# Performance work log

Hardware: AMD Instinct MI355X
Metric: run time of the kernel (lower is better)

Reference implementation:

```python
import jax, jax.numpy as jnp
import numpy as np

DOT_TEMP = 0.05  # hardcoded in the original forward (self.temperature is never used)
EPS = 1e-6


def setup_inputs() -> dict:
    key = jax.random.key(0)
    k1, k2 = jax.random.split(key)
    bsz, n_views, dim = 4096, 2, 128
    features = jax.random.normal(k1, (bsz, n_views, dim), dtype=jnp.float32)
    labels = jax.random.randint(k2, (bsz,), 0, 100, dtype=jnp.int32)
    return {"features": features, "labels": labels}


def reference(features, labels):
    bsz, V, dim = features.shape  # V = n_views; contrast_mode='all' -> anchor_count = contrast_count = V
    n = V * bsz

    # contrast_feature = cat(unbind(features, dim=1), dim=0): [view0 batch; view1 batch; ...]
    cf = jnp.transpose(features, (1, 0, 2)).reshape(n, dim)  # [n, dim]

    # positive mask: eq(labels, labels.T) tiled, diagonal zeroed
    eq = labels[:, None] == labels[None, :]  # [bsz, bsz]
    mask = jnp.tile(eq.astype(jnp.float32), (V, V))  # [n, n]
    mask = mask * (1.0 - jnp.eye(n, dtype=jnp.float32))

    # Key simplification (exactly faithful): mask3[i] (eq) and mask2[i] (ne) are complementary,
    # so unique(cat(where(mask3[i]), where(mask2[i]))) == arange(n) for every row. Hence each
    # loop iteration in the original computes the SAME scalar from the full gram matrix.
    lab2 = jnp.tile(labels, V)  # matches labels2[:n] layout in the original
    diff = (lab2[:, None] != lab2[None, :]).astype(jnp.float32)  # [n, n]

    dots = jnp.matmul(cf, cf.T) / DOT_TEMP  # [n, n]
    dm = dots * diff
    maxd = jnp.max(dm, axis=1, keepdims=True)
    S = jnp.sum(jnp.exp(dm - maxd))  # exp_terms.sum() -- identical for every valid row
    N = jnp.sum(diff)                # different_label_mask.sum()

    # rows with mask2[i].sum() == 0 are skipped (left at zero)
    valid = jnp.tile(jnp.any(labels[None, :] != labels[:, None], axis=1), V)  # [n]
    xv = jnp.where(valid, S, 0.0)
    nv = jnp.where(valid, N, 0.0)

    # if not all(negtivesum == 0): x = x / negtivesum   (safe divide for skipped rows)
    all_zero = jnp.all(nv == 0.0)
    xv = jnp.where(all_zero, xv, xv / jnp.where(nv == 0.0, 1.0, nv))

    log_prob = -jnp.log(xv[:, None] + EPS)  # [n, 1], broadcast over columns
    msum = jnp.sum(mask, axis=1)
    msum_safe = jnp.where(msum == 0.0, 1.0, msum)
    pos_logits = -jnp.sum(mask * log_prob, axis=1) / msum_safe  # [n]
    loss = jnp.mean(pos_logits)  # mean over view(anchor_count, bsz) == overall mean
    return loss
```

## Files before the change

### kernel.cpp

```cpp
#include <hip/hip_runtime.h>
#include <hip/hip_bf16.h>
#include <stdint.h>

#define N_TOT 8192
#define BSZ   4096
#define NCH   32
#define SCALE2 28.853900817779268f

typedef _Float16 f16x8 __attribute__((ext_vector_type(8)));
typedef float f32x4 __attribute__((ext_vector_type(4)));

__device__ __forceinline__ float fast_exp2(float x) {
#if __has_builtin(__builtin_amdgcn_exp2f)
  return __builtin_amdgcn_exp2f(x);
#else
  return exp2f(x);
#endif
}
#define EXP2(x) fast_exp2(x)

__global__ __launch_bounds__(256) void prep13_kernel(
    const float* __restrict__ feat, const int* __restrict__ labels,
    _Float16* __restrict__ H2, unsigned char* __restrict__ lab8, int* __restrict__ cnt) {
  if (blockIdx.x == 512) {
    __shared__ int h[128];
    if (threadIdx.x < 128) h[threadIdx.x] = 0;
    __syncthreads();
    for (int i = threadIdx.x; i < BSZ; i += 256) atomicAdd(&h[labels[i] & 127], 1);
    __syncthreads();
    if (threadIdx.x < 128) cnt[threadIdx.x] = h[threadIdx.x];
    for (int i = threadIdx.x; i < N_TOT; i += 256)
      lab8[i] = (unsigned char)labels[i & (BSZ - 1)];
    return;
  }
  int idx = blockIdx.x * 256 + threadIdx.x;
  int rowblk = idx >> 8, inner = idx & 255;
  int k8 = inner >> 4, rlo = inner & 15;
  int r = rowblk * 16 + rlo;
  int b = r & (BSZ - 1), v = r >> 12;
  const float* src = feat + ((size_t)((b << 1) + v) << 7) + k8 * 8;
  float4 x0 = *(const float4*)src;
  float4 x1 = *(const float4*)(src + 4);
  float xs[8] = {x0.x, x0.y, x0.z, x0.w, x1.x, x1.y, x1.z, x1.w};
  f16x8 hv;
#pragma unroll
  for (int j = 0; j < 8; ++j) hv[j] = (_Float16)xs[j];
  *(f16x8*)((char*)H2 + (size_t)idx * 16) = hv;
}

__global__ __launch_bounds__(256) void gemm13_kernel(
    const _Float16* __restrict__ H2, const int* __restrict__ labels,
    const unsigned char* __restrict__ lab8,
    float* __restrict__ pM, float* __restrict__ pS) {
  int orig = blockIdx.x;
  int xcd = orig & 7, j = orig >> 3;
  int cg = xcd * 4 + (j & 3);
  int sp = j >> 2;
  int wave = threadIdx.x >> 6, lane = threadIdx.x & 63;
  int strip = sp * 4 + wave;
  int lq = lane >> 4, lr16 = lane & 15;

  const uint32_t rowbase = (uint32_t)strip * 32;
  const char* Hb = (const char*)H2;
  const uint32_t laneoff = lq * 256 + lr16 * 16;

  int lrw[2];
#pragma unroll
  for (int m = 0; m < 2; ++m)
    lrw[m] = labels[(rowbase + m * 16 + lr16) & (BSZ - 1)];

  f16x8 Areg[2][4];
#pragma unroll
  for (int m = 0; m < 2; ++m)
#pragma unroll
    for (int kb = 0; kb < 4; ++kb)
      Areg[m][kb] = *(const f16x8*)(Hb + (size_t)((rowbase >> 4) + m) * 4096 + kb * 1024 + laneoff);
#pragma unroll
  for (int m = 0; m < 2; ++m)
#pragma unroll
    for (int kb = 0; kb < 4; ++kb)
      Areg[m][kb] = Areg[m][kb] * (_Float16)SCALE2;

  const char* Bbase = Hb + (size_t)cg * 65536;

#define BLOAD(T, NI, KB) \
  (*(const f16x8*)(Bbase + ((T) * 4 + (NI)) * 4096 + (KB) * 1024 + laneoff))

  f32x4 acc[2][4];
  float mxv[2] = {-3.0e38f, -3.0e38f}, sv[2] = {0.0f, 0.0f};

  f16x8 Bb[2][4];
#pragma unroll
  for (int ni = 0; ni < 4; ++ni) Bb[0][ni] = BLOAD(0, ni, 0);

#pragma unroll
  for (int t = 0; t < 4; ++t) {
#pragma unroll
    for (int m = 0; m < 2; ++m)
#pragma unroll
      for (int ni = 0; ni < 4; ++ni) acc[m][ni] = f32x4{0.f, 0.f, 0.f, 0.f};
    uint32_t labw[4];
#pragma unroll
    for (int ni = 0; ni < 4; ++ni)
      labw[ni] = *(const uint32_t*)(lab8 + cg * 256 + t * 64 + ni * 16 + lq * 4);

#pragma unroll
    for (int kb = 0; kb < 4; ++kb) {
      int cur = kb & 1;
      if (kb < 3) {
#pragma unroll
        for (int ni = 0; ni < 4; ++ni) Bb[cur ^ 1][ni] = BLOAD(t, ni, kb + 1);
      } else if (t < 3) {
#pragma unroll
        for (int ni = 0; ni < 4; ++ni) Bb[cur ^ 1][ni] = BLOAD(t + 1, ni, 0);
      }
      __builtin_amdgcn_s_setprio(1);
#pragma unroll
      for (int m = 0; m < 2; ++m)
#pragma unroll
        for (int ni = 0; ni < 4; ++ni)
          acc[m][ni] = __builtin_amdgcn_mfma_f32_16x16x32_f16(Bb[cur][ni], Areg[m][kb], acc[m][ni], 0, 0, 0);
      __builtin_amdgcn_s_setprio(0);
    }

#pragma unroll
    for (int m = 0; m < 2; ++m) {
#pragma unroll
      for (int ni = 0; ni < 4; ++ni)
#pragma unroll
        for (int r = 0; r < 4; ++r) {
          int lc = (labw[ni] >> (8 * r)) & 255;
          acc[m][ni][r] = (lrw[m] != lc) ? acc[m][ni][r] : 0.0f;
        }
      float b0 = fmaxf(fmaxf(acc[m][0][0], acc[m][0][1]), fmaxf(acc[m][0][2], acc[m][0][3]));
      float b1 = fmaxf(fmaxf(acc[m][1][0], acc[m][1][1]), fmaxf(acc[m][1][2], acc[m][1][3]));
      float b2 = fmaxf(fmaxf(acc[m][2][0], acc[m][2][1]), fmaxf(acc[m][2][2], acc[m][2][3]));
      float b3 = fmaxf(fmaxf(acc[m][3][0], acc[m][3][1]), fmaxf(acc[m][3][2], acc[m][3][3]));
      float bm = fmaxf(fmaxf(b0, b1), fmaxf(b2, b3));
      float nm = fmaxf(mxv[m], bm);
      float s0 = 0.f, s1 = 0.f, s2 = 0.f, s3 = 0.f;
#pragma unroll
      for (int r = 0; r < 4; ++r) {
        s0 += EXP2(acc[m][0][r] - nm);
        s1 += EXP2(acc[m][1][r] - nm);
        s2 += EXP2(acc[m][2][r] - nm);
        s3 += EXP2(acc[m][3][r] - nm);
      }
      sv[m] = sv[m] * EXP2(mxv[m] - nm) + ((s0 + s1) + (s2 + s3));
      mxv[m] = nm;
    }
  }
#undef BLOAD

#pragma unroll
  for (int m = 0; m < 2; ++m) {
    float M = mxv[m], S = sv[m];
#pragma unroll
    for (int off = 16; off < 64; off <<= 1) {
      float Mo = __shfl_xor(M, off, 64);
      float So = __shfl_xor(S, off, 64);
      float Mn = fmaxf(M, Mo);
      S = S * EXP2(M - Mn) + So * EXP2(Mo - Mn);
      M = Mn;
    }
    if (lane < 16) {
      pM[(size_t)cg * N_TOT + rowbase + m * 16 + lane] = M;
      pS[(size_t)cg * N_TOT + rowbase + m * 16 + lane] = S;
    }
  }
}

__global__ __launch_bounds__(256) void rowred13_kernel(const float* __restrict__ pM,
                                                       const float* __restrict__ pS,
                                                       float* __restrict__ blockS) {
  int row = blockIdx.x * 256 + threadIdx.x;
  float M = -3.0e38f;
#pragma unroll
  for (int c = 0; c < NCH; ++c) M = fmaxf(M, pM[(size_t)c * N_TOT + row]);
  float s = 0.0f;
#pragma unroll
  for (int c = 0; c < NCH; ++c)
    s += pS[(size_t)c * N_TOT + row] * EXP2(pM[(size_t)c * N_TOT + row] - M);
  __shared__ float red[256];
  red[threadIdx.x] = s;
  __syncthreads();
  for (int st = 128; st > 0; st >>= 1) {
    if (threadIdx.x < st) red[threadIdx.x] += red[threadIdx.x + st];
    __syncthreads();
  }
  if (threadIdx.x == 0) blockS[blockIdx.x] = red[0];
}

__global__ void final13_kernel(const float* __restrict__ blockS, const int* __restrict__ cnt,
                               float* __restrict__ out) {
  int lane = threadIdx.x;
  float s = (lane < 32) ? blockS[lane] : 0.0f;
#pragma unroll
  for (int off = 1; off < 64; off <<= 1) s += __shfl_xor(s, off, 64);
  if (lane == 0) {
    double Stot = (double)s;
    long long sumsq = 0;
    int nval = 0;
    for (int c = 0; c < 128; ++c) {
      long long cc = cnt[c];
      sumsq += cc * cc;
      if (cc > 0 && cc < BSZ) nval += 2 * (int)cc;
    }
    double Nd = (double)N_TOT * (double)N_TOT - 4.0 * (double)sumsq;
    float loss;
    if (Nd <= 0.0 || nval == 0) {
      loss = logf(1e-6f);
    } else {
      float x = (float)(Stot / Nd);
      loss = ((float)nval * logf(x + 1e-6f) +
              (float)(N_TOT - nval) * logf(1e-6f)) / (float)N_TOT;
    }
    out[0] = loss;
  }
}

extern "C" void kernel_launch(void* const* d_in, const int* in_sizes, int n_in,
                              void* d_out, int out_size, void* d_ws, size_t ws_size,
                              hipStream_t stream) {
  const float* feat = (const float*)d_in[0];
  const int* labels = (const int*)d_in[1];
  float* out = (float*)d_out;

  char* ws = (char*)d_ws;
  _Float16* H2        = (_Float16*)(ws);
  unsigned char* lab8 = (unsigned char*)(ws + 2097152);
  float* pM           = (float*)(ws + 2105344);
  float* pS           = (float*)(ws + 3153920);
  int* cnt            = (int*)(ws + 4202496);
  float* blockS       = (float*)(ws + 4203008);

  prep13_kernel<<<513, 256, 0, stream>>>(feat, labels, H2, lab8, cnt);
  gemm13_kernel<<<2048, 256, 0, stream>>>(H2, labels, lab8, pM, pS);
  rowred13_kernel<<<32, 256, 0, stream>>>(pM, pS, blockS);
  final13_kernel<<<1, 64, 0, stream>>>(blockS, cnt, out);
}
```

Before: 50.48 us.

## Stage shared B tiles in LDS via async global_load_lds and fold scale into prep

```diff
diff --git a/kernel.cpp b/kernel.cpp
--- a/kernel.cpp
+++ b/kernel.cpp
@@ -5,7 +5,7 @@
 #define N_TOT 8192
 #define BSZ   4096
 #define NCH   32
-#define SCALE2 28.853900817779268f
+#define SQS   5.3715827f
 
 typedef _Float16 f16x8 __attribute__((ext_vector_type(8)));
 typedef float f32x4 __attribute__((ext_vector_type(4)));
@@ -19,7 +19,7 @@
 }
 #define EXP2(x) fast_exp2(x)
 
-__global__ __launch_bounds__(256) void prep13_kernel(
+__global__ __launch_bounds__(256) void prep14_kernel(
     const float* __restrict__ feat, const int* __restrict__ labels,
     _Float16* __restrict__ H2, unsigned char* __restrict__ lab8, int* __restrict__ cnt) {
   if (blockIdx.x == 512) {
@@ -44,23 +44,24 @@
   float xs[8] = {x0.x, x0.y, x0.z, x0.w, x1.x, x1.y, x1.z, x1.w};
   f16x8 hv;
 #pragma unroll
-  for (int j = 0; j < 8; ++j) hv[j] = (_Float16)xs[j];
+  for (int jj = 0; jj < 8; ++jj) hv[jj] = (_Float16)(xs[jj] * SQS);
   *(f16x8*)((char*)H2 + (size_t)idx * 16) = hv;
 }
 
-__global__ __launch_bounds__(256) void gemm13_kernel(
+__global__ __launch_bounds__(256) void gemm14_kernel(
     const _Float16* __restrict__ H2, const int* __restrict__ labels,
     const unsigned char* __restrict__ lab8,
     float* __restrict__ pM, float* __restrict__ pS) {
+  __shared__ __align__(16) char ldsB[2][16384];
+
   int orig = blockIdx.x;
   int xcd = orig & 7, j = orig >> 3;
   int cg = xcd * 4 + (j & 3);
-  int sp = j >> 2;
+  int rg = j >> 2;
   int wave = threadIdx.x >> 6, lane = threadIdx.x & 63;
-  int strip = sp * 4 + wave;
   int lq = lane >> 4, lr16 = lane & 15;
 
-  const uint32_t rowbase = (uint32_t)strip * 32;
+  const uint32_t rowbase = (uint32_t)rg * 128 + wave * 32;
   const char* Hb = (const char*)H2;
   const uint32_t laneoff = lq * 256 + lr16 * 16;
 
@@ -75,82 +76,99 @@
 #pragma unroll
     for (int kb = 0; kb < 4; ++kb)
       Areg[m][kb] = *(const f16x8*)(Hb + (size_t)((rowbase >> 4) + m) * 4096 + kb * 1024 + laneoff);
-#pragma unroll
-  for (int m = 0; m < 2; ++m)
-#pragma unroll
-    for (int kb = 0; kb < 4; ++kb)
-      Areg[m][kb] = Areg[m][kb] * (_Float16)SCALE2;
-
-  const char* Bbase = Hb + (size_t)cg * 65536;
-
-#define BLOAD(T, NI, KB) \
-  (*(const f16x8*)(Bbase + ((T) * 4 + (NI)) * 4096 + (KB) * 1024 + laneoff))
+
+  const char* Bsrc = Hb + (size_t)cg * 65536;
+
+#define STAGE(T, BUF)                                                                     \
+  {                                                                                       \
+    _Pragma("unroll")                                                                     \
+    for (int i = 0; i < 4; ++i) {                                                         \
+      int chunk = wave * 4 + i;                                                           \
+      __builtin_amdgcn_global_load_lds(                                                   \
+          (const __attribute__((address_space(1))) void*)(Bsrc + ((T) * 4 + (chunk >> 2)) * 4096 + (chunk & 3) * 1024 + lane * 16), \
+          (__attribute__((address_space(3))) void*)(&ldsB[BUF][chunk * 1024]), 16, 0, 0); \
+    }                                                                                     \
+  }
+
+  STAGE(0, 0);
+  asm volatile("s_waitcnt vmcnt(0)" ::: "memory");
+  __builtin_amdgcn_sched_barrier(0);
+  __builtin_amdgcn_s_barrier();
 
   f32x4 acc[2][4];
   float mxv[2] = {-3.0e38f, -3.0e38f}, sv[2] = {0.0f, 0.0f};
 
-  f16x8 Bb[2][4];
-#pragma unroll
-  for (int ni = 0; ni < 4; ++ni) Bb[0][ni] = BLOAD(0, ni, 0);
-
 #pragma unroll
   for (int t = 0; t < 4; ++t) {
+    if (t < 3) STAGE(t + 1, (t + 1) & 1);
+    const char* Bb = ldsB[t & 1];
+
 #pragma unroll
     for (int m = 0; m < 2; ++m)
 #pragma unroll
       for (int ni = 0; ni < 4; ++ni) acc[m][ni] = f32x4{0.f, 0.f, 0.f, 0.f};
-    uint32_t labw[4];
+
+    f16x8 Bf[2][4];
 #pragma unroll
     for (int ni = 0; ni < 4; ++ni)
-      labw[ni] = *(const uint32_t*)(lab8 + cg * 256 + t * 64 + ni * 16 + lq * 4);
-
+      Bf[0][ni] = *(const f16x8*)(Bb + ni * 4096 + laneoff);
 #pragma unroll
     for (int kb = 0; kb < 4; ++kb) {
       int cur = kb & 1;
       if (kb < 3) {
 #pragma unroll
-        for (int ni = 0; ni < 4; ++ni) Bb[cur ^ 1][ni] = BLOAD(t, ni, kb + 1);
-      } else if (t < 3) {
-#pragma unroll
-        for (int ni = 0; ni < 4; ++ni) Bb[cur ^ 1][ni] = BLOAD(t + 1, ni, 0);
+        for (int ni = 0; ni < 4; ++ni)
+          Bf[cur ^ 1][ni] = *(const f16x8*)(Bb + ni * 4096 + (kb + 1) * 1024 + laneoff);
       }
       __builtin_amdgcn_s_setprio(1);
 #pragma unroll
       for (int m = 0; m < 2; ++m)
 #pragma unroll
         for (int ni = 0; ni < 4; ++ni)
-          acc[m][ni] = __builtin_amdgcn_mfma_f32_16x16x32_f16(Bb[cur][ni], Areg[m][kb], acc[m][ni], 0, 0, 0);
+          acc[m][ni] = __builtin_amdgcn_mfma_f32_16x16x32_f16(Bf[cur][ni], Areg[m][kb], acc[m][ni], 0, 0, 0);
       __builtin_amdgcn_s_setprio(0);
     }
 
+    uint32_t labw[4];
+#pragma unroll
+    for (int ni = 0; ni < 4; ++ni)
+      labw[ni] = *(const uint32_t*)(lab8 + cg * 256 + t * 64 + ni * 16 + lq * 4);
+    int lc[16];
+#pragma unroll
+    for (int i = 0; i < 16; ++i) lc[i] = (labw[i >> 2] >> (8 * (i & 3))) & 255;
+
 #pragma unroll
     for (int m = 0; m < 2; ++m) {
+      float v[16];
 #pragma unroll
       for (int ni = 0; ni < 4; ++ni)
 #pragma unroll
-        for (int r = 0; r < 4; ++r) {
-          int lc = (labw[ni] >> (8 * r)) & 255;
-          acc[m][ni][r] = (lrw[m] != lc) ? acc[m][ni][r] : 0.0f;
-        }
-      float b0 = fmaxf(fmaxf(acc[m][0][0], acc[m][0][1]), fmaxf(acc[m][0][2], acc[m][0][3]));
-      float b1 = fmaxf(fmaxf(acc[m][1][0], acc[m][1][1]), fmaxf(acc[m][1][2], acc[m][1][3]));
-      float b2 = fmaxf(fmaxf(acc[m][2][0], acc[m][2][1]), fmaxf(acc[m][2][2], acc[m][2][3]));
-      float b3 = fmaxf(fmaxf(acc[m][3][0], acc[m][3][1]), fmaxf(acc[m][3][2], acc[m][3][3]));
-      float bm = fmaxf(fmaxf(b0, b1), fmaxf(b2, b3));
+        for (int r = 0; r < 4; ++r)
+          v[ni * 4 + r] = (lrw[m] != lc[ni * 4 + r]) ? acc[m][ni][r] : 0.0f;
+      float m01 = fmaxf(v[0], v[1]),  m23 = fmaxf(v[2], v[3]);
+      float m45 = fmaxf(v[4], v[5]),  m67 = fmaxf(v[6], v[7]);
+      float m89 = fmaxf(v[8], v[9]),  mab = fmaxf(v[10], v[11]);
+      float mcd = fmaxf(v[12], v[13]), mef = fmaxf(v[14], v[15]);
+      float bm = fmaxf(fmaxf(fmaxf(m01, m23), fmaxf(m45, m67)),
+                       fmaxf(fmaxf(m89, mab), fmaxf(mcd, mef)));
       float nm = fmaxf(mxv[m], bm);
       float s0 = 0.f, s1 = 0.f, s2 = 0.f, s3 = 0.f;
 #pragma unroll
       for (int r = 0; r < 4; ++r) {
-        s0 += EXP2(acc[m][0][r] - nm);
-        s1 += EXP2(acc[m][1][r] - nm);
-        s2 += EXP2(acc[m][2][r] - nm);
-        s3 += EXP2(acc[m][3][r] - nm);
+        s0 += EXP2(v[r] - nm);
+        s1 += EXP2(v[4 + r] - nm);
+        s2 += EXP2(v[8 + r] - nm);
+        s3 += EXP2(v[12 + r] - nm);
       }
       sv[m] = sv[m] * EXP2(mxv[m] - nm) + ((s0 + s1) + (s2 + s3));
       mxv[m] = nm;
     }
-  }
-#undef BLOAD
+
+    asm volatile("s_waitcnt vmcnt(0)" ::: "memory");
+    __builtin_amdgcn_sched_barrier(0);
+    __builtin_amdgcn_s_barrier();
+  }
+#undef STAGE
 
 #pragma unroll
   for (int m = 0; m < 2; ++m) {
@@ -170,7 +188,7 @@
   }
 }
 
-__global__ __launch_bounds__(256) void rowred13_kernel(const float* __restrict__ pM,
+__global__ __launch_bounds__(256) void rowred14_kernel(const float* __restrict__ pM,
                                                        const float* __restrict__ pS,
                                                        float* __restrict__ blockS) {
   int row = blockIdx.x * 256 + threadIdx.x;
@@ -191,7 +209,7 @@
   if (threadIdx.x == 0) blockS[blockIdx.x] = red[0];
 }
 
-__global__ void final13_kernel(const float* __restrict__ blockS, const int* __restrict__ cnt,
+__global__ void final14_kernel(const float* __restrict__ blockS, const int* __restrict__ cnt,
                                float* __restrict__ out) {
   int lane = threadIdx.x;
   float s = (lane < 32) ? blockS[lane] : 0.0f;
@@ -234,8 +252,8 @@
   int* cnt            = (int*)(ws + 4202496);
   float* blockS       = (float*)(ws + 4203008);
 
-  prep13_kernel<<<513, 256, 0, stream>>>(feat, labels, H2, lab8, cnt);
-  gemm13_kernel<<<2048, 256, 0, stream>>>(H2, labels, lab8, pM, pS);
-  rowred13_kernel<<<32, 256, 0, stream>>>(pM, pS, blockS);
-  final13_kernel<<<1, 64, 0, stream>>>(blockS, cnt, out);
-}
+  prep14_kernel<<<513, 256, 0, stream>>>(feat, labels, H2, lab8, cnt);
+  gemm14_kernel<<<2048, 256, 0, stream>>>(H2, labels, lab8, pM, pS);
+  rowred14_kernel<<<32, 256, 0, stream>>>(pM, pS, blockS);
+  final14_kernel<<<1, 64, 0, stream>>>(blockS, cnt, out);
+}
```

Measured after the change: 46.07 us. 8.7% less time.
